# Kernel optimization log

Measured on AMD Instinct MI355X. Metric: run time of the kernel, lower is better.

The kernel has to match this reference:

```python
import jax, jax.numpy as jnp
import numpy as np

OD, OH, OW = 4, 8, 8
PAD = 1


def _adaptive_max_1d(x, axis, out_size):
    """PyTorch AdaptiveMaxPool rule along one axis: window i = [floor(i*n/o), ceil((i+1)*n/o))."""
    n = x.shape[axis]
    outs = []
    for i in range(out_size):  # tiny static loop (<=8)
        s = (i * n) // out_size
        e = -((-(i + 1) * n) // out_size)  # ceil((i+1)*n/o)
        outs.append(jnp.max(jax.lax.slice_in_dim(x, s, e, axis=axis), axis=axis, keepdims=True))
    return jnp.concatenate(outs, axis=axis)


def setup_inputs() -> dict:
    key = jax.random.key(0)
    k1, k2, k3, k4 = jax.random.split(key, 4)
    C = 32
    x = jax.random.normal(k1, (8, C, 32, 128, 128), dtype=jnp.float32)
    bound = 1.0 / np.sqrt(C)
    W_proj = jax.random.uniform(k2, (C, C), dtype=jnp.float32, minval=-bound, maxval=bound)
    W_final = jax.random.uniform(k3, (C, C), dtype=jnp.float32, minval=-bound, maxval=bound)
    b_final = jax.random.uniform(k4, (C,), dtype=jnp.float32, minval=-bound, maxval=bound)
    return {"x": x, "W_proj": W_proj, "W_final": W_final, "b_final": b_final}


def reference(x, W_proj, W_final, b_final):
    # ReflectionPad3d(pad=1) on the last three dims
    xp = jnp.pad(x, ((0, 0), (0, 0), (PAD, PAD), (PAD, PAD), (PAD, PAD)), mode="reflect")
    # AdaptiveMaxPool3d to (OD, OH, OW), applied separably per axis (max is separable)
    p = _adaptive_max_1d(xp, 2, OD)
    p = _adaptive_max_1d(p, 3, OH)
    p = _adaptive_max_1d(p, 4, OW)  # (B, C, OD, OH, OW)
    B, C = p.shape[0], p.shape[1]
    S = OD * OH * OW
    x_feat = p.transpose(0, 2, 3, 4, 1).reshape(B, S, C)       # (B, S, C)
    x_proj = jnp.einsum("bsc,dc->bsd", x_feat, W_proj)          # Linear, no bias
    context = x_proj.mean(axis=1)                               # (B, C)
    att_logits = jnp.einsum("bc,bsc->bs", context, x_proj)      # (B, S)
    # logsoftmax followed by exp == softmax (numerically stable)
    att_weights = jax.nn.softmax(att_logits, axis=1)
    weighted = jnp.einsum("bs,bsc->bc", att_weights, x_proj)    # (B, C)
    channel_logits = weighted @ W_final.T + b_final
    return jax.nn.log_softmax(channel_logits, axis=1)
```

## Files before the change

kernel.cpp:

```cpp
#include <hip/hip_runtime.h>
#include <cfloat>
#include <cmath>


__device__ inline unsigned fkey(float f) {
    unsigned u = __float_as_uint(f);
    return (u & 0x80000000u) ? ~u : (u | 0x80000000u);
}
__device__ inline float funkey(unsigned k) {
    return __uint_as_float((k & 0x80000000u) ? (k ^ 0x80000000u) : ~k);
}
__device__ inline float max4(float4 v) { return fmaxf(fmaxf(v.x, v.y), fmaxf(v.z, v.w)); }

__global__ __launch_bounds__(256) void pool_kernel(const float* __restrict__ x,
                                                   float* __restrict__ pooled) {
    const int blk = blockIdx.x;
    const int g_h = blk & 1;
    const int g_d = (blk >> 1) & 1;
    const int bc  = blk >> 2;
    const int t    = threadIdx.x;
    const int j    = t & 7;
    const int rowg = t >> 3;

    __shared__ unsigned accK[2][4][8];
    if (t < 64) ((unsigned*)accK)[t] = 0u;
    __syncthreads();

    const float* px = x + ((size_t)bc * 32 + (size_t)g_d * 16) * (128 * 128)
                        + (size_t)(g_h * 64 + rowg) * 128 + j * 16;
    const int lim = 7 + g_d;

    float a0m0 = -FLT_MAX, a0m1 = -FLT_MAX;
    float a1m0 = -FLT_MAX, a1m1 = -FLT_MAX;

    #pragma unroll 2
    for (int dl = 0; dl < 16; ++dl) {
        const float4* p0 = (const float4*)(px + (size_t)dl * (128 * 128));
        const float4* p1 = (const float4*)(px + (size_t)dl * (128 * 128) + 32 * 128);
        float4 u0 = p0[0], u1 = p0[1], u2 = p0[2], u3 = p0[3];
        float4 w0 = p1[0], w1 = p1[1], w2 = p1[2], w3 = p1[3];

        float cmax0 = fmaxf(fmaxf(max4(u0), max4(u1)), fmaxf(max4(u2), max4(u3)));
        float cmax1 = fmaxf(fmaxf(max4(w0), max4(w1)), fmaxf(max4(w2), max4(w3)));

        float nl0 = __shfl_up(u3.w, 1, 8);
        float nf0 = __shfl_down(u0.x, 1, 8);
        float nl1 = __shfl_up(w3.w, 1, 8);
        float nf1 = __shfl_down(w0.x, 1, 8);
        if (j >= 1 && j <= 3) { cmax0 = fmaxf(cmax0, nl0); cmax1 = fmaxf(cmax1, nl1); }
        if (j >= 4 && j <= 6) { cmax0 = fmaxf(cmax0, nf0); cmax1 = fmaxf(cmax1, nf1); }

        const bool m0 = (dl <= lim), m1 = (dl >= lim);
        if (m0) { a0m0 = fmaxf(a0m0, cmax0); a1m0 = fmaxf(a1m0, cmax1); }
        if (m1) { a0m1 = fmaxf(a0m1, cmax0); a1m1 = fmaxf(a1m1, cmax1); }
    }

    {
        const int rl0 = rowg, rl1 = 32 + rowg;
        const int ohl0 = rl0 >> 4, ohl1 = rl1 >> 4;
        unsigned k00 = fkey(a0m0), k01 = fkey(a0m1);
        unsigned k10 = fkey(a1m0), k11 = fkey(a1m1);
        atomicMax(&accK[0][ohl0][j], k00);
        atomicMax(&accK[1][ohl0][j], k01);
        atomicMax(&accK[0][ohl1][j], k10);
        atomicMax(&accK[1][ohl1][j], k11);
        if (g_h == 0) {
            if ((rl0 & 15) == 15) {
                atomicMax(&accK[0][ohl0 + 1][j], k00);
                atomicMax(&accK[1][ohl0 + 1][j], k01);
            }
            if ((rl1 & 15) == 15 && rl1 != 63) {
                atomicMax(&accK[0][ohl1 + 1][j], k10);
                atomicMax(&accK[1][ohl1 + 1][j], k11);
            }
        } else {
            if ((rl0 & 15) == 0 && rl0 != 0) {
                atomicMax(&accK[0][ohl0 - 1][j], k00);
                atomicMax(&accK[1][ohl0 - 1][j], k01);
            }
            if ((rl1 & 15) == 0) {
                atomicMax(&accK[0][ohl1 - 1][j], k10);
                atomicMax(&accK[1][ohl1 - 1][j], k11);
            }
        }
    }
    __syncthreads();

    if (t < 64) {
        const int odl = t >> 5, ohl = (t >> 3) & 3, ow = t & 7;
        float v = funkey(accK[odl][ohl][ow]);
        const int b = bc >> 5, c = bc & 31;
        const int s = (g_d * 2 + odl) * 64 + (g_h * 4 + ohl) * 8 + ow;
        pooled[((size_t)b * 256 + s) * 32 + c] = v;
    }
}

__global__ __launch_bounds__(256) void attn_kernel(const float* __restrict__ pooled,
                                                   const float* __restrict__ Wp,
                                                   const float* __restrict__ Wf,
                                                   const float* __restrict__ bfin,
                                                   float* __restrict__ out) {
    const int b = blockIdx.x;
    const int t = threadIdx.x;
    const int lane = t & 63, wave = t >> 6;
    __shared__ float sWp[1024];
    __shared__ float part[4][32];
    __shared__ float sctx[32];
    __shared__ float sw[32];
    __shared__ float red[4];

    for (int i = t; i < 1024; i += 256) sWp[i] = Wp[i];
    __syncthreads();

    float xf[32];
    #pragma unroll
    for (int c2 = 0; c2 < 32; ++c2) xf[c2] = pooled[(size_t)b * 8192 + t * 32 + c2];

    float xp[32];
    #pragma unroll
    for (int d2 = 0; d2 < 32; ++d2) {
        float s = 0.f;
        #pragma unroll
        for (int c2 = 0; c2 < 32; ++c2) s += xf[c2] * sWp[d2 * 32 + c2];
        xp[d2] = s;
    }

    #pragma unroll
    for (int d2 = 0; d2 < 32; ++d2) {
        float v = xp[d2];
        for (int off = 32; off >= 1; off >>= 1) v += __shfl_xor(v, off, 64);
        if (lane == 0) part[wave][d2] = v;
    }
    __syncthreads();
    if (t < 32) sctx[t] = (part[0][t] + part[1][t] + part[2][t] + part[3][t]) * (1.0f / 256.0f);
    __syncthreads();

    float l = 0.f;
    #pragma unroll
    for (int c2 = 0; c2 < 32; ++c2) l += sctx[c2] * xp[c2];
    float v = l;
    for (int off = 32; off >= 1; off >>= 1) v = fmaxf(v, __shfl_xor(v, off, 64));
    if (lane == 0) red[wave] = v;
    __syncthreads();
    const float M = fmaxf(fmaxf(red[0], red[1]), fmaxf(red[2], red[3]));
    const float e = expf(l - M);
    v = e;
    for (int off = 32; off >= 1; off >>= 1) v += __shfl_xor(v, off, 64);
    __syncthreads();
    if (lane == 0) red[wave] = v;
    __syncthreads();
    const float S = red[0] + red[1] + red[2] + red[3];
    const float att = e / S;

    #pragma unroll
    for (int d2 = 0; d2 < 32; ++d2) {
        float w = att * xp[d2];
        for (int off = 32; off >= 1; off >>= 1) w += __shfl_xor(w, off, 64);
        if (lane == 0) part[wave][d2] = w;
    }
    __syncthreads();
    if (t < 32) sw[t] = part[0][t] + part[1][t] + part[2][t] + part[3][t];
    __syncthreads();

    if (t < 32) {
        float logit = bfin[t];
        #pragma unroll
        for (int k = 0; k < 32; ++k) logit += sw[k] * Wf[t * 32 + k];
        float m2 = logit;
        for (int off = 16; off >= 1; off >>= 1) m2 = fmaxf(m2, __shfl_xor(m2, off, 32));
        const float e2 = expf(logit - m2);
        float s2 = e2;
        for (int off = 16; off >= 1; off >>= 1) s2 += __shfl_xor(s2, off, 32);
        out[b * 32 + t] = logit - m2 - logf(s2);
    }
}

extern "C" void kernel_launch(void* const* d_in, const int* in_sizes, int n_in,
                              void* d_out, int out_size, void* d_ws, size_t ws_size,
                              hipStream_t stream) {
    const float* x  = (const float*)d_in[0];
    const float* Wp = (const float*)d_in[1];
    const float* Wf = (const float*)d_in[2];
    const float* bf = (const float*)d_in[3];
    float* out = (float*)d_out;
    float* pooled = (float*)d_ws;

    pool_kernel<<<dim3(1024), dim3(256), 0, stream>>>(x, pooled);
    attn_kernel<<<dim3(8), dim3(256), 0, stream>>>(pooled, Wp, Wf, bf, out);
}
```

Baseline: 764.8 us.

## Remap pool threads to coalesced float4 columns with per-thread row accumulators

Each thread now owns one float4 column across eight strided rows, so consecutive lanes read consecutive 16-byte chunks and global loads are fully coalesced. The old layout had each thread read 64 contiguous bytes with scattered lanes. Window boundary handling moves from cross-lane shuffles to per-thread edge accumulators for the columns and rows that straddle windows. This adds more registers and more shared-memory atomics at the end, since there are now 8 atomics per thread plus extra ones for edge lanes.

Measured after the change: 767.2 us. About the same (+0.3%).

```diff
diff --git a/kernel.cpp b/kernel.cpp
--- a/kernel.cpp
+++ b/kernel.cpp
@@ -18,80 +18,79 @@
     const int g_h = blk & 1;
     const int g_d = (blk >> 1) & 1;
     const int bc  = blk >> 2;
-    const int t    = threadIdx.x;
-    const int j    = t & 7;
-    const int rowg = t >> 3;
+    const int t = threadIdx.x;
+    const int c = t & 31;
+    const int r = t >> 5;
 
     __shared__ unsigned accK[2][4][8];
     if (t < 64) ((unsigned*)accK)[t] = 0u;
-    __syncthreads();
 
-    const float* px = x + ((size_t)bc * 32 + (size_t)g_d * 16) * (128 * 128)
-                        + (size_t)(g_h * 64 + rowg) * 128 + j * 16;
+    const float4* px = (const float4*)(x + ((size_t)bc * 32 + (size_t)g_d * 16) * 16384
+                                         + (size_t)g_h * 64 * 128)
+                       + (size_t)(r * 32 + c);
     const int lim = 7 + g_d;
 
-    float a0m0 = -FLT_MAX, a0m1 = -FLT_MAX;
-    float a1m0 = -FLT_MAX, a1m1 = -FLT_MAX;
+    const bool hasW = (c == 3 || c == 7 || c == 11);
+    const bool hasX = (c == 20 || c == 24 || c == 28);
+    const bool hasE = hasW || hasX;
 
-    #pragma unroll 2
+    float accA[4], accB[4], eA[4], eB[4];
+    #pragma unroll
+    for (int i = 0; i < 4; ++i) { accA[i] = -FLT_MAX; accB[i] = -FLT_MAX;
+                                  eA[i]   = -FLT_MAX; eB[i]   = -FLT_MAX; }
+
     for (int dl = 0; dl < 16; ++dl) {
-        const float4* p0 = (const float4*)(px + (size_t)dl * (128 * 128));
-        const float4* p1 = (const float4*)(px + (size_t)dl * (128 * 128) + 32 * 128);
-        float4 u0 = p0[0], u1 = p0[1], u2 = p0[2], u3 = p0[3];
-        float4 w0 = p1[0], w1 = p1[1], w2 = p1[2], w3 = p1[3];
+        const float4* p = px + (size_t)dl * 4096;
+        float4 v[8];
+        #pragma unroll
+        for (int k = 0; k < 8; ++k) v[k] = p[k * 256];
+        const bool m0 = (dl <= lim), m1 = (dl >= lim);
 
-        float cmax0 = fmaxf(fmaxf(max4(u0), max4(u1)), fmaxf(max4(u2), max4(u3)));
-        float cmax1 = fmaxf(fmaxf(max4(w0), max4(w1)), fmaxf(max4(w2), max4(w3)));
+        #pragma unroll
+        for (int k = 0; k < 8; ++k) {
+            const int oh = k >> 1;
+            const float m  = max4(v[k]);
+            const float ev = hasW ? v[k].w : v[k].x;
+            if (m0) { accA[oh] = fmaxf(accA[oh], m); if (hasE) eA[oh] = fmaxf(eA[oh], ev); }
+            if (m1) { accB[oh] = fmaxf(accB[oh], m); if (hasE) eB[oh] = fmaxf(eB[oh], ev); }
 
-        float nl0 = __shfl_up(u3.w, 1, 8);
-        float nf0 = __shfl_down(u0.x, 1, 8);
-        float nl1 = __shfl_up(w3.w, 1, 8);
-        float nf1 = __shfl_down(w0.x, 1, 8);
-        if (j >= 1 && j <= 3) { cmax0 = fmaxf(cmax0, nl0); cmax1 = fmaxf(cmax1, nl1); }
-        if (j >= 4 && j <= 6) { cmax0 = fmaxf(cmax0, nf0); cmax1 = fmaxf(cmax1, nf1); }
-
-        const bool m0 = (dl <= lim), m1 = (dl >= lim);
-        if (m0) { a0m0 = fmaxf(a0m0, cmax0); a1m0 = fmaxf(a1m0, cmax1); }
-        if (m1) { a0m1 = fmaxf(a0m1, cmax0); a1m1 = fmaxf(a1m1, cmax1); }
-    }
-
-    {
-        const int rl0 = rowg, rl1 = 32 + rowg;
-        const int ohl0 = rl0 >> 4, ohl1 = rl1 >> 4;
-        unsigned k00 = fkey(a0m0), k01 = fkey(a0m1);
-        unsigned k10 = fkey(a1m0), k11 = fkey(a1m1);
-        atomicMax(&accK[0][ohl0][j], k00);
-        atomicMax(&accK[1][ohl0][j], k01);
-        atomicMax(&accK[0][ohl1][j], k10);
-        atomicMax(&accK[1][ohl1][j], k11);
-        if (g_h == 0) {
-            if ((rl0 & 15) == 15) {
-                atomicMax(&accK[0][ohl0 + 1][j], k00);
-                atomicMax(&accK[1][ohl0 + 1][j], k01);
-            }
-            if ((rl1 & 15) == 15 && rl1 != 63) {
-                atomicMax(&accK[0][ohl1 + 1][j], k10);
-                atomicMax(&accK[1][ohl1 + 1][j], k11);
-            }
-        } else {
-            if ((rl0 & 15) == 0 && rl0 != 0) {
-                atomicMax(&accK[0][ohl0 - 1][j], k00);
-                atomicMax(&accK[1][ohl0 - 1][j], k01);
-            }
-            if ((rl1 & 15) == 0) {
-                atomicMax(&accK[0][ohl1 - 1][j], k10);
-                atomicMax(&accK[1][ohl1 - 1][j], k11);
+            if (g_h == 0) {
+                if ((k & 1) == 1 && k < 7 && r == 7) {
+                    if (m0) { accA[oh+1] = fmaxf(accA[oh+1], m); if (hasE) eA[oh+1] = fmaxf(eA[oh+1], ev); }
+                    if (m1) { accB[oh+1] = fmaxf(accB[oh+1], m); if (hasE) eB[oh+1] = fmaxf(eB[oh+1], ev); }
+                }
+            } else {
+                if ((k & 1) == 0 && k > 0 && r == 0) {
+                    if (m0) { accA[oh-1] = fmaxf(accA[oh-1], m); if (hasE) eA[oh-1] = fmaxf(eA[oh-1], ev); }
+                    if (m1) { accB[oh-1] = fmaxf(accB[oh-1], m); if (hasE) eB[oh-1] = fmaxf(eB[oh-1], ev); }
+                }
             }
         }
     }
     __syncthreads();
 
+    const int ow = c >> 2;
+    #pragma unroll
+    for (int oh = 0; oh < 4; ++oh) {
+        atomicMax(&accK[0][oh][ow], fkey(accA[oh]));
+        atomicMax(&accK[1][oh][ow], fkey(accB[oh]));
+    }
+    if (hasE) {
+        const int owe = hasW ? (ow + 1) : (ow - 1);
+        #pragma unroll
+        for (int oh = 0; oh < 4; ++oh) {
+            atomicMax(&accK[0][oh][owe], fkey(eA[oh]));
+            atomicMax(&accK[1][oh][owe], fkey(eB[oh]));
+        }
+    }
+    __syncthreads();
+
     if (t < 64) {
-        const int odl = t >> 5, ohl = (t >> 3) & 3, ow = t & 7;
-        float v = funkey(accK[odl][ohl][ow]);
-        const int b = bc >> 5, c = bc & 31;
-        const int s = (g_d * 2 + odl) * 64 + (g_h * 4 + ohl) * 8 + ow;
-        pooled[((size_t)b * 256 + s) * 32 + c] = v;
+        const int odl = t >> 5, ohl = (t >> 3) & 3, oww = t & 7;
+        const float v = funkey(accK[odl][ohl][oww]);
+        const int b = bc >> 5, ch = bc & 31;
+        const int s = (g_d * 2 + odl) * 64 + (g_h * 4 + ohl) * 8 + oww;
+        pooled[((size_t)b * 256 + s) * 32 + ch] = v;
     }
 }
 
```
